# Optimization experiments

Hardware: AMD Instinct MI355X
Metric: run time of the kernel (lower is better)

## Reference

```python
import jax, jax.numpy as jnp
import numpy as np

IN_DIM = 3
GRID_LEVEL = 7
FEAT_DIMS = 2
HIDDEN = 128
BOUND = 1.0
W0_SINE = 56.0  # n_levels**feature_dims - n_levels = 8**2 - 8
N = 131072


def setup_inputs() -> dict:
    key = jax.random.key(0)
    ks = jax.random.split(key, 10)
    return {
        "in_pos": jax.random.uniform(ks[0], (N, IN_DIM), jnp.float32, -1.0, 1.0),
        "grid_feats": jax.random.uniform(ks[1], (N, IN_DIM + GRID_LEVEL * FEAT_DIMS), jnp.float32),
        "ffn_A": jax.random.normal(ks[2], (GRID_LEVEL, FEAT_DIMS, HIDDEN), jnp.float32) * 5.0,
        "ffn_sigma": jnp.ones((GRID_LEVEL,), jnp.float32),
        "W0": jax.random.uniform(ks[3], (HIDDEN, IN_DIM), jnp.float32, -1.0 / IN_DIM, 1.0 / IN_DIM),
        "b0": jax.random.uniform(ks[4], (HIDDEN,), jnp.float32, -1.0 / IN_DIM, 1.0 / IN_DIM),
        "W_mid": jax.random.uniform(ks[5], (GRID_LEVEL, HIDDEN, HIDDEN), jnp.float32) * (2.0 * np.sqrt(6.0 / HIDDEN) / W0_SINE) - np.sqrt(6.0 / HIDDEN) / W0_SINE,
        "b_mid": jnp.zeros((GRID_LEVEL, HIDDEN), jnp.float32),
        "W_high": jax.random.uniform(ks[6], (GRID_LEVEL, HIDDEN, HIDDEN), jnp.float32) * (2.0 * np.sqrt(6.0 / HIDDEN) / W0_SINE) - np.sqrt(6.0 / HIDDEN) / W0_SINE,
        "b_high": jnp.zeros((GRID_LEVEL, HIDDEN), jnp.float32),
    }


def reference(in_pos, grid_feats, ffn_A, ffn_sigma, W0, b0, W_mid, b_mid, W_high, b_high):
    x = in_pos / BOUND                     # [N, 3], in [-1, 1]
    pos01 = (in_pos + BOUND) / (2.0 * BOUND)  # [N, 3], in [0, 1]

    # grid branch: slice off the first in_dim columns, reshape to [L, N, F]
    gx = grid_feats[..., IN_DIM:].reshape(-1, GRID_LEVEL, FEAT_DIMS).transpose(1, 0, 2)
    A = ffn_A * ffn_sigma[:, None, None]   # [L, F, H]
    grid_x = jnp.sin(jnp.einsum('lnf,lfh->lnh', gx, (2.0 * jnp.pi) * A))  # [L, N, H]

    # first SIREN layer
    x = jnp.sin(W0_SINE * (x @ W0.T + b0))  # [N, H]

    def step(carry, layer):
        x, buf = carry
        Wm, bm, Wh, bh, g = layer
        x = jnp.sin(W0_SINE * (x @ Wm.T + bm))
        x = g + x                                  # residual add of grid features
        buf = buf + jnp.sin(W0_SINE * (x @ Wh.T + bh))  # high-freq accumulation
        return (x, buf), None

    buf0 = jnp.zeros((x.shape[0], HIDDEN), x.dtype)
    (_, buf), _ = jax.lax.scan(step, (x, buf0), (W_mid, b_mid, W_high, b_high, grid_x))

    return jnp.concatenate([pos01, buf / GRID_LEVEL], axis=-1)  # [N, 3 + 128]
```

## Files before the change

### kernel.cpp

```cpp
#include <hip/hip_runtime.h>
#include <hip/hip_bf16.h>


typedef __bf16 bf16_t;
typedef __attribute__((ext_vector_type(8))) __bf16 bf16x8;
typedef __attribute__((ext_vector_type(4))) float f32x4;
typedef __attribute__((ext_vector_type(16))) float f32x16;

#define C56R 8.9126768f
#define INV7 0.14285714285714285f

#define OFF_WMF   0
#define OFF_WMFLO 229376
#define OFF_WHF   458752
#define OFF_EPM   688128

union ChunkU { bf16x8 v; unsigned int d[4]; };

__device__ __forceinline__ unsigned short bfbits(float x) {
  bf16_t b = (bf16_t)x;
  return __builtin_bit_cast(unsigned short, b);
}
__device__ __forceinline__ float bf2f(unsigned short u) {
  return __builtin_bit_cast(float, (unsigned int)u << 16);
}
__device__ __forceinline__ void pack2(float v0, float v1,
                                      unsigned int& ph, unsigned int& pl) {
  unsigned short h0 = bfbits(v0), h1 = bfbits(v1);
  ph = (unsigned int)h0 | ((unsigned int)h1 << 16);
  float l0 = v0 - bf2f(h0), l1 = v1 - bf2f(h1);
  pl = (unsigned int)bfbits(l0) | ((unsigned int)bfbits(l1) << 16);
}
__device__ __forceinline__ void stage16(const void* g, void* l) {
  __builtin_amdgcn_global_load_lds(
      (const __attribute__((address_space(1))) unsigned int*)g,
      (__attribute__((address_space(3))) unsigned int*)l, 16, 0, 0);
}

__global__ void ffb_prep(const float* __restrict__ ffnA, const float* __restrict__ sigma,
                         const float* __restrict__ Wm, const float* __restrict__ bm,
                         const float* __restrict__ Wh, const float* __restrict__ bh,
                         unsigned char* __restrict__ ws) {
  int i = blockIdx.x * 256 + threadIdx.x;
  bf16_t* wmf = (bf16_t*)(ws + OFF_WMF);
  bf16_t* wml = (bf16_t*)(ws + OFF_WMFLO);
  bf16_t* whf = (bf16_t*)(ws + OFF_WHF);
  {
    int j    = i & 7;
    int lane = (i >> 3) & 63;
    int kc   = (i >> 9) & 7;
    int mt   = (i >> 12) & 3;
    int it   = i >> 14;
    int ho   = (mt << 5) + (lane & 31);
    int hin  = (kc << 4) + ((lane >> 5) << 3) + j;
    int src  = (it << 14) + (ho << 7) + hin;
    float w  = Wm[src];
    bf16_t h = (bf16_t)w;
    wmf[i] = h;
    wml[i] = (bf16_t)(w - (float)h);
    whf[i] = (bf16_t)Wh[src];
  }
  if (i < 896) {
    int r  = i & 15;
    int mt = (i >> 4) & 3;
    int hf = (i >> 6) & 1;
    int it = i >> 7;
    int h  = (mt << 5) + (r & 3) + ((r >> 2) << 3) + (hf << 2);
    float sg = sigma[it];
    f32x4 e;
    e.x = ffnA[it * 256 + h] * sg;
    e.y = ffnA[it * 256 + 128 + h] * sg;
    e.z = C56R * bm[it * 128 + h];
    e.w = C56R * bh[it * 128 + h];
    ((f32x4*)(ws + OFF_EPM))[i] = e;
  }
}

__launch_bounds__(512, 4)
__global__ void ffb_main(const float* __restrict__ pos,
                         const float* __restrict__ gfeat,
                         const float* __restrict__ W0,
                         const float* __restrict__ b0,
                         const unsigned char* __restrict__ ws,
                         float* __restrict__ out) {
  __shared__ __align__(16) unsigned char smem[65536];

  const int tid  = threadIdx.x;
  const int L    = tid & 63;
  const int wave = tid >> 6;
  const int qd   = wave >> 2;
  const int sub  = wave & 3;
  const int p    = L & 31;
  const int hf   = L >> 5;
  const int n    = (blockIdx.x << 6) + (qd << 5) + p;

  unsigned char* sMH = smem;
  unsigned char* sX  = smem + 32768 + (qd << 14);

  const bf16_t* __restrict__ WML = (const bf16_t*)(ws + OFF_WMFLO);
  const bf16_t* __restrict__ WHF = (const bf16_t*)(ws + OFF_WHF);
  const f32x4*  __restrict__ EPM = (const f32x4*)(ws + OFF_EPM);
  const float*  __restrict__ EPW = (const float*)(ws + OFF_EPM);

  {
    const unsigned char* src = ws + OFF_WMF + (wave << 12) + (L << 4);
    unsigned char* dst = sMH + (wave << 12);
    #pragma unroll
    for (int c = 0; c < 4; ++c)
      stage16(src + (c << 10), dst + (c << 10));
  }

  const float p0 = pos[n * 3 + 0], p1 = pos[n * 3 + 1], p2 = pos[n * 3 + 2];
  if (sub == 0 && hf == 0) {
    out[n * 131 + 0] = (p0 + 1.f) * 0.5f;
    out[n * 131 + 1] = (p1 + 1.f) * 0.5f;
    out[n * 131 + 2] = (p2 + 1.f) * 0.5f;
  }

  #pragma unroll
  for (int cc = 0; cc < 2; ++cc) {
    const int c = (sub << 1) + cc;
    ChunkU chi, clo;
    #pragma unroll
    for (int jp = 0; jp < 4; ++jp) {
      int h0 = (c << 4) + (hf << 3) + 2 * jp;
      float d0 = __builtin_fmaf(p2, W0[h0*3+2], __builtin_fmaf(p1, W0[h0*3+1], p0 * W0[h0*3+0]));
      float d1 = __builtin_fmaf(p2, W0[h0*3+5], __builtin_fmaf(p1, W0[h0*3+4], p0 * W0[h0*3+3]));
      float v0 = __builtin_amdgcn_sinf(C56R * (d0 + b0[h0]));
      float v1 = __builtin_amdgcn_sinf(C56R * (d1 + b0[h0 + 1]));
      pack2(v0, v1, chi.d[jp], clo.d[jp]);
    }
    *(bf16x8*)(sX + (c << 10) + (L << 4))        = chi.v;
    *(bf16x8*)(sX + 8192 + (c << 10) + (L << 4)) = clo.v;
  }
  __syncthreads();

  f32x16 buf;
  #pragma unroll
  for (int r = 0; r < 16; ++r) buf[r] = 0.f;

  for (int it = 0; it < 8; ++it) {
    if (it > 0) {
      f32x16 acc;
      #pragma unroll
      for (int r = 0; r < 16; ++r) acc[r] = 0.f;
      const bf16_t* wb = WHF + ((it - 1) << 14) + (sub << 12) + (L << 3);
      bf16x8 fnext = *(const bf16x8*)(wb);
      #pragma unroll
      for (int kc = 0; kc < 8; ++kc) {
        bf16x8 f = fnext;
        if (kc < 7) fnext = *(const bf16x8*)(wb + ((kc + 1) << 9));
        bf16x8 xhc = *(const bf16x8*)(sX + (kc << 10) + (L << 4));
        acc = __builtin_amdgcn_mfma_f32_32x32x16_bf16(f, xhc, acc, 0, 0, 0);
      }
      const int eb = ((((it - 1) << 1) + hf) << 2) + sub;
      #pragma unroll
      for (int r = 0; r < 16; ++r) {
        float cbh = EPW[(eb * 16 + r) * 4 + 3];
        buf[r] += __builtin_amdgcn_sinf(__builtin_fmaf(acc[r], C56R, cbh));
      }
    }

    if (it < 7) {
      f32x16 acc;
      #pragma unroll
      for (int r = 0; r < 16; ++r) acc[r] = 0.f;
      const bf16_t* wl = WML + (it << 14) + (sub << 12) + (L << 3);
      const unsigned char* smh = sMH + (sub << 13) + (L << 4);
      bf16x8 flnext = *(const bf16x8*)(wl);
      #pragma unroll
      for (int kc = 0; kc < 8; ++kc) {
        bf16x8 fl = flnext;
        if (kc < 7) flnext = *(const bf16x8*)(wl + ((kc + 1) << 9));
        bf16x8 fh  = *(const bf16x8*)(smh + (kc << 10));
        bf16x8 xhc = *(const bf16x8*)(sX + (kc << 10) + (L << 4));
        bf16x8 xlc = *(const bf16x8*)(sX + 8192 + (kc << 10) + (L << 4));
        acc = __builtin_amdgcn_mfma_f32_32x32x16_bf16(fh, xhc, acc, 0, 0, 0);
        acc = __builtin_amdgcn_mfma_f32_32x32x16_bf16(fl, xhc, acc, 0, 0, 0);
        acc = __builtin_amdgcn_mfma_f32_32x32x16_bf16(fh, xlc, acc, 0, 0, 0);
      }

      __syncthreads();

      if (it < 6) {
        const unsigned char* src = ws + OFF_WMF + ((it + 1) << 15) + (wave << 12) + (L << 4);
        unsigned char* dst = sMH + (wave << 12);
        #pragma unroll
        for (int c = 0; c < 4; ++c)
          stage16(src + (c << 10), dst + (c << 10));
      }

      const float g0 = gfeat[n * 17 + 3 + 2 * it];
      const float g1 = gfeat[n * 17 + 4 + 2 * it];
      const int eb = (((it << 1) + hf) << 2) + sub;
      #pragma unroll
      for (int rp = 0; rp < 8; ++rp) {
        const int r = 2 * rp;
        f32x4 e0 = EPM[eb * 16 + r];
        f32x4 e1 = EPM[eb * 16 + r + 1];
        float sg0 = __builtin_amdgcn_sinf(__builtin_amdgcn_fractf(__builtin_fmaf(g1, e0.y, g0 * e0.x)));
        float sg1 = __builtin_amdgcn_sinf(__builtin_amdgcn_fractf(__builtin_fmaf(g1, e1.y, g0 * e1.x)));
        float sm0 = __builtin_amdgcn_sinf(__builtin_fmaf(acc[r],     C56R, e0.z));
        float sm1 = __builtin_amdgcn_sinf(__builtin_fmaf(acc[r + 1], C56R, e1.z));
        unsigned int phv, plv;
        pack2(sg0 + sm0, sg1 + sm1, phv, plv);
        const int h   = (sub << 5) + (r & 3) + ((r >> 2) << 3) + (hf << 2);
        const int off = ((h >> 4) << 10) + ((p + (((h >> 3) & 1) << 5)) << 4) + ((h & 7) << 1);
        *(unsigned int*)(sX + off)        = phv;
        *(unsigned int*)(sX + 8192 + off) = plv;
      }
      __syncthreads();
    }
  }

  float* op = out + (size_t)n * 131 + 3;
  #pragma unroll
  for (int r = 0; r < 16; ++r) {
    const int h = (sub << 5) + (r & 3) + ((r >> 2) << 3) + (hf << 2);
    op[h] = buf[r] * INV7;
  }
}

extern "C" void kernel_launch(void* const* d_in, const int* in_sizes, int n_in,
                              void* d_out, int out_size, void* d_ws, size_t ws_size,
                              hipStream_t stream) {
  (void)in_sizes; (void)n_in; (void)out_size; (void)ws_size;
  const float* pos   = (const float*)d_in[0];
  const float* gfeat = (const float*)d_in[1];
  const float* ffnA  = (const float*)d_in[2];
  const float* sigma = (const float*)d_in[3];
  const float* W0    = (const float*)d_in[4];
  const float* b0    = (const float*)d_in[5];
  const float* Wm    = (const float*)d_in[6];
  const float* bm    = (const float*)d_in[7];
  const float* Wh    = (const float*)d_in[8];
  const float* bh    = (const float*)d_in[9];
  float* out = (float*)d_out;
  unsigned char* ws = (unsigned char*)d_ws;

  hipLaunchKernelGGL(ffb_prep, dim3(448), dim3(256), 0, stream,
                     ffnA, sigma, Wm, bm, Wh, bh, ws);
  hipLaunchKernelGGL(ffb_main, dim3(2048), dim3(512), 0, stream,
                     pos, gfeat, W0, b0, ws, out);
}
```

Measured before the change: 284.3 us.

## Keep activations in registers with each wave owning all output rows for 32 points

Each wave now computes all 128 hidden outputs for its own 32 points, so the activations stay in registers across layers instead of round-tripping through shared memory. The hi and lo mid-layer weights are both staged in LDS, and the bf16 activation fragments are rebuilt with permlane32 swaps between lanes. Blocks now cover 256 points, so the grid drops to 512 blocks and occupancy is lowered to 2 blocks per CU. The cost is much higher register pressure (four accumulators plus the x fragments and buf), which may cause spills or lower occupancy.

```diff
diff --git a/kernel.cpp b/kernel.cpp
--- a/kernel.cpp
+++ b/kernel.cpp
@@ -76,148 +76,164 @@
   }
 }
 
-__launch_bounds__(512, 4)
+__launch_bounds__(512, 2)
 __global__ void ffb_main(const float* __restrict__ pos,
                          const float* __restrict__ gfeat,
                          const float* __restrict__ W0,
                          const float* __restrict__ b0,
                          const unsigned char* __restrict__ ws,
                          float* __restrict__ out) {
-  __shared__ __align__(16) unsigned char smem[65536];
+  __shared__ __align__(16) unsigned char sW[65536];
 
   const int tid  = threadIdx.x;
   const int L    = tid & 63;
   const int wave = tid >> 6;
-  const int qd   = wave >> 2;
-  const int sub  = wave & 3;
   const int p    = L & 31;
   const int hf   = L >> 5;
-  const int n    = (blockIdx.x << 6) + (qd << 5) + p;
-
-  unsigned char* sMH = smem;
-  unsigned char* sX  = smem + 32768 + (qd << 14);
-
-  const bf16_t* __restrict__ WML = (const bf16_t*)(ws + OFF_WMFLO);
+  const int n    = (blockIdx.x << 8) + (wave << 5) + p;
+
   const bf16_t* __restrict__ WHF = (const bf16_t*)(ws + OFF_WHF);
   const f32x4*  __restrict__ EPM = (const f32x4*)(ws + OFF_EPM);
   const float*  __restrict__ EPW = (const float*)(ws + OFF_EPM);
 
   {
-    const unsigned char* src = ws + OFF_WMF + (wave << 12) + (L << 4);
-    unsigned char* dst = sMH + (wave << 12);
-    #pragma unroll
-    for (int c = 0; c < 4; ++c)
-      stage16(src + (c << 10), dst + (c << 10));
+    const unsigned char* srcb = ws + (wave < 4 ? OFF_WMF : OFF_WMFLO)
+                              + ((wave & 3) << 13) + (L << 4);
+    unsigned char* dstb = sW + ((wave >> 2) << 15) + ((wave & 3) << 13);
+    #pragma unroll
+    for (int c = 0; c < 8; ++c)
+      stage16(srcb + (c << 10), dstb + (c << 10));
   }
 
   const float p0 = pos[n * 3 + 0], p1 = pos[n * 3 + 1], p2 = pos[n * 3 + 2];
-  if (sub == 0 && hf == 0) {
-    out[n * 131 + 0] = (p0 + 1.f) * 0.5f;
-    out[n * 131 + 1] = (p1 + 1.f) * 0.5f;
-    out[n * 131 + 2] = (p2 + 1.f) * 0.5f;
-  }
-
+  if (hf == 0) {
+    out[(size_t)n * 131 + 0] = (p0 + 1.f) * 0.5f;
+    out[(size_t)n * 131 + 1] = (p1 + 1.f) * 0.5f;
+    out[(size_t)n * 131 + 2] = (p2 + 1.f) * 0.5f;
+  }
+
+  bf16x8 xh[8], xl[8];
   #pragma unroll
-  for (int cc = 0; cc < 2; ++cc) {
-    const int c = (sub << 1) + cc;
+  for (int kc = 0; kc < 8; ++kc) {
     ChunkU chi, clo;
     #pragma unroll
     for (int jp = 0; jp < 4; ++jp) {
-      int h0 = (c << 4) + (hf << 3) + 2 * jp;
+      const int h0 = (kc << 4) + (hf << 3) + 2 * jp;
       float d0 = __builtin_fmaf(p2, W0[h0*3+2], __builtin_fmaf(p1, W0[h0*3+1], p0 * W0[h0*3+0]));
       float d1 = __builtin_fmaf(p2, W0[h0*3+5], __builtin_fmaf(p1, W0[h0*3+4], p0 * W0[h0*3+3]));
       float v0 = __builtin_amdgcn_sinf(C56R * (d0 + b0[h0]));
       float v1 = __builtin_amdgcn_sinf(C56R * (d1 + b0[h0 + 1]));
       pack2(v0, v1, chi.d[jp], clo.d[jp]);
     }
-    *(bf16x8*)(sX + (c << 10) + (L << 4))        = chi.v;
-    *(bf16x8*)(sX + 8192 + (c << 10) + (L << 4)) = clo.v;
-  }
+    xh[kc] = chi.v;
+    xl[kc] = clo.v;
+  }
+
+  f32x16 buf[4];
+  #pragma unroll
+  for (int mt = 0; mt < 4; ++mt)
+    #pragma unroll
+    for (int r = 0; r < 16; ++r) buf[mt][r] = 0.f;
+
   __syncthreads();
 
-  f32x16 buf;
-  #pragma unroll
-  for (int r = 0; r < 16; ++r) buf[r] = 0.f;
-
-  for (int it = 0; it < 8; ++it) {
-    if (it > 0) {
-      f32x16 acc;
-      #pragma unroll
-      for (int r = 0; r < 16; ++r) acc[r] = 0.f;
-      const bf16_t* wb = WHF + ((it - 1) << 14) + (sub << 12) + (L << 3);
-      bf16x8 fnext = *(const bf16x8*)(wb);
-      #pragma unroll
-      for (int kc = 0; kc < 8; ++kc) {
-        bf16x8 f = fnext;
-        if (kc < 7) fnext = *(const bf16x8*)(wb + ((kc + 1) << 9));
-        bf16x8 xhc = *(const bf16x8*)(sX + (kc << 10) + (L << 4));
-        acc = __builtin_amdgcn_mfma_f32_32x32x16_bf16(f, xhc, acc, 0, 0, 0);
-      }
-      const int eb = ((((it - 1) << 1) + hf) << 2) + sub;
+  #pragma unroll 1
+  for (int l = 0; l < 7; ++l) {
+    f32x16 acc[4];
+    #pragma unroll
+    for (int mt = 0; mt < 4; ++mt)
+      #pragma unroll
+      for (int r = 0; r < 16; ++r) acc[mt][r] = 0.f;
+
+    #pragma unroll
+    for (int kc = 0; kc < 8; ++kc) {
+      #pragma unroll
+      for (int mt = 0; mt < 4; ++mt) {
+        const bf16x8 fh = *(const bf16x8*)(sW + (mt << 13) + (kc << 10) + (L << 4));
+        const bf16x8 fl = *(const bf16x8*)(sW + 32768 + (mt << 13) + (kc << 10) + (L << 4));
+        acc[mt] = __builtin_amdgcn_mfma_f32_32x32x16_bf16(fh, xh[kc], acc[mt], 0, 0, 0);
+        acc[mt] = __builtin_amdgcn_mfma_f32_32x32x16_bf16(fl, xh[kc], acc[mt], 0, 0, 0);
+        acc[mt] = __builtin_amdgcn_mfma_f32_32x32x16_bf16(fh, xl[kc], acc[mt], 0, 0, 0);
+      }
+    }
+    __syncthreads();
+
+    if (l < 6) {
+      const unsigned char* srcb = ws + (wave < 4 ? OFF_WMF : OFF_WMFLO)
+                                + ((l + 1) << 15) + ((wave & 3) << 13) + (L << 4);
+      unsigned char* dstb = sW + ((wave >> 2) << 15) + ((wave & 3) << 13);
+      #pragma unroll
+      for (int c = 0; c < 8; ++c)
+        stage16(srcb + (c << 10), dstb + (c << 10));
+    }
+
+    const float g0 = gfeat[n * 17 + 3 + 2 * l];
+    const float g1 = gfeat[n * 17 + 4 + 2 * l];
+    #pragma unroll
+    for (int mt = 0; mt < 4; ++mt) {
+      const int eb = (((l << 1) + hf) << 2) + mt;
+      float v[16];
       #pragma unroll
       for (int r = 0; r < 16; ++r) {
-        float cbh = EPW[(eb * 16 + r) * 4 + 3];
-        buf[r] += __builtin_amdgcn_sinf(__builtin_fmaf(acc[r], C56R, cbh));
-      }
-    }
-
-    if (it < 7) {
-      f32x16 acc;
-      #pragma unroll
-      for (int r = 0; r < 16; ++r) acc[r] = 0.f;
-      const bf16_t* wl = WML + (it << 14) + (sub << 12) + (L << 3);
-      const unsigned char* smh = sMH + (sub << 13) + (L << 4);
-      bf16x8 flnext = *(const bf16x8*)(wl);
-      #pragma unroll
-      for (int kc = 0; kc < 8; ++kc) {
-        bf16x8 fl = flnext;
-        if (kc < 7) flnext = *(const bf16x8*)(wl + ((kc + 1) << 9));
-        bf16x8 fh  = *(const bf16x8*)(smh + (kc << 10));
-        bf16x8 xhc = *(const bf16x8*)(sX + (kc << 10) + (L << 4));
-        bf16x8 xlc = *(const bf16x8*)(sX + 8192 + (kc << 10) + (L << 4));
-        acc = __builtin_amdgcn_mfma_f32_32x32x16_bf16(fh, xhc, acc, 0, 0, 0);
-        acc = __builtin_amdgcn_mfma_f32_32x32x16_bf16(fl, xhc, acc, 0, 0, 0);
-        acc = __builtin_amdgcn_mfma_f32_32x32x16_bf16(fh, xlc, acc, 0, 0, 0);
-      }
-
-      __syncthreads();
-
-      if (it < 6) {
-        const unsigned char* src = ws + OFF_WMF + ((it + 1) << 15) + (wave << 12) + (L << 4);
-        unsigned char* dst = sMH + (wave << 12);
-        #pragma unroll
-        for (int c = 0; c < 4; ++c)
-          stage16(src + (c << 10), dst + (c << 10));
-      }
-
-      const float g0 = gfeat[n * 17 + 3 + 2 * it];
-      const float g1 = gfeat[n * 17 + 4 + 2 * it];
-      const int eb = (((it << 1) + hf) << 2) + sub;
-      #pragma unroll
-      for (int rp = 0; rp < 8; ++rp) {
-        const int r = 2 * rp;
-        f32x4 e0 = EPM[eb * 16 + r];
-        f32x4 e1 = EPM[eb * 16 + r + 1];
-        float sg0 = __builtin_amdgcn_sinf(__builtin_amdgcn_fractf(__builtin_fmaf(g1, e0.y, g0 * e0.x)));
-        float sg1 = __builtin_amdgcn_sinf(__builtin_amdgcn_fractf(__builtin_fmaf(g1, e1.y, g0 * e1.x)));
-        float sm0 = __builtin_amdgcn_sinf(__builtin_fmaf(acc[r],     C56R, e0.z));
-        float sm1 = __builtin_amdgcn_sinf(__builtin_fmaf(acc[r + 1], C56R, e1.z));
-        unsigned int phv, plv;
-        pack2(sg0 + sm0, sg1 + sm1, phv, plv);
-        const int h   = (sub << 5) + (r & 3) + ((r >> 2) << 3) + (hf << 2);
-        const int off = ((h >> 4) << 10) + ((p + (((h >> 3) & 1) << 5)) << 4) + ((h & 7) << 1);
-        *(unsigned int*)(sX + off)        = phv;
-        *(unsigned int*)(sX + 8192 + off) = plv;
-      }
-      __syncthreads();
-    }
+        const f32x4 e = EPM[eb * 16 + r];
+        const float sg = __builtin_amdgcn_sinf(__builtin_amdgcn_fractf(__builtin_fmaf(g1, e.y, g0 * e.x)));
+        const float sm = __builtin_amdgcn_sinf(__builtin_fmaf(acc[mt][r], C56R, e.z));
+        v[r] = sg + sm;
+      }
+      #pragma unroll
+      for (int bh = 0; bh < 2; ++bh) {
+        unsigned int Ah, Al, Bh, Bl, Ch, Cl, Dh, Dl;
+        pack2(v[8*bh + 0], v[8*bh + 1], Ah, Al);
+        pack2(v[8*bh + 2], v[8*bh + 3], Bh, Bl);
+        pack2(v[8*bh + 4], v[8*bh + 5], Ch, Cl);
+        pack2(v[8*bh + 6], v[8*bh + 7], Dh, Dl);
+        asm("v_permlane32_swap_b32 %0, %1" : "+v"(Ah), "+v"(Ch));
+        asm("v_permlane32_swap_b32 %0, %1" : "+v"(Bh), "+v"(Dh));
+        asm("v_permlane32_swap_b32 %0, %1" : "+v"(Al), "+v"(Cl));
+        asm("v_permlane32_swap_b32 %0, %1" : "+v"(Bl), "+v"(Dl));
+        ChunkU uh, ul;
+        uh.d[0] = Ah; uh.d[1] = Bh; uh.d[2] = Ch; uh.d[3] = Dh;
+        ul.d[0] = Al; ul.d[1] = Bl; ul.d[2] = Cl; ul.d[3] = Dl;
+        xh[2*mt + bh] = uh.v;
+        xl[2*mt + bh] = ul.v;
+      }
+    }
+
+    f32x16 hac[4];
+    #pragma unroll
+    for (int mt = 0; mt < 4; ++mt)
+      #pragma unroll
+      for (int r = 0; r < 16; ++r) hac[mt][r] = 0.f;
+
+    const bf16_t* whb = WHF + (l << 14) + (L << 3);
+    #pragma unroll
+    for (int kc = 0; kc < 8; ++kc) {
+      #pragma unroll
+      for (int mt = 0; mt < 4; ++mt) {
+        const bf16x8 f = *(const bf16x8*)(whb + (mt << 12) + (kc << 9));
+        hac[mt] = __builtin_amdgcn_mfma_f32_32x32x16_bf16(f, xh[kc], hac[mt], 0, 0, 0);
+      }
+    }
+    #pragma unroll
+    for (int mt = 0; mt < 4; ++mt) {
+      const int eb = (((l << 1) + hf) << 2) + mt;
+      #pragma unroll
+      for (int r = 0; r < 16; ++r) {
+        const float cbh = EPW[(eb * 16 + r) * 4 + 3];
+        buf[mt][r] += __builtin_amdgcn_sinf(__builtin_fmaf(hac[mt][r], C56R, cbh));
+      }
+    }
+    __syncthreads();
   }
 
   float* op = out + (size_t)n * 131 + 3;
   #pragma unroll
-  for (int r = 0; r < 16; ++r) {
-    const int h = (sub << 5) + (r & 3) + ((r >> 2) << 3) + (hf << 2);
-    op[h] = buf[r] * INV7;
+  for (int mt = 0; mt < 4; ++mt) {
+    #pragma unroll
+    for (int r = 0; r < 16; ++r) {
+      const int h = (mt << 5) + (r & 3) + ((r >> 2) << 3) + (hf << 2);
+      op[h] = buf[mt][r] * INV7;
+    }
   }
 }
 
@@ -240,6 +256,6 @@
 
   hipLaunchKernelGGL(ffb_prep, dim3(448), dim3(256), 0, stream,
                      ffnA, sigma, Wm, bm, Wh, bh, ws);
-  hipLaunchKernelGGL(ffb_main, dim3(2048), dim3(512), 0, stream,
+  hipLaunchKernelGGL(ffb_main, dim3(512), dim3(512), 0, stream,
                      pos, gfeat, W0, b0, ws, out);
 }
```

Measured after the change: 369.2 us. 29.9% more time.

## Drop LDS staging of mid-layer weights and halve block size

Applied to the files above, without the earlier changes.

Removes the async global-to-LDS staging of the high-part mid-layer weights and loads them directly from global memory into registers with a one-step register prefetch, like the low part. Blocks shrink from 512 to 256 threads (one 32-point group per block), LDS drops from 64KB to 16KB, and the launch bound moves to 8 blocks per CU to raise occupancy. This trades the LDS weight sharing across two point groups for more global/L2 weight traffic per block and extra register pressure from the second prefetch stream.

```diff
diff --git a/kernel.cpp b/kernel.cpp
--- a/kernel.cpp
+++ b/kernel.cpp
@@ -30,11 +30,6 @@
   ph = (unsigned int)h0 | ((unsigned int)h1 << 16);
   float l0 = v0 - bf2f(h0), l1 = v1 - bf2f(h1);
   pl = (unsigned int)bfbits(l0) | ((unsigned int)bfbits(l1) << 16);
-}
-__device__ __forceinline__ void stage16(const void* g, void* l) {
-  __builtin_amdgcn_global_load_lds(
-      (const __attribute__((address_space(1))) unsigned int*)g,
-      (__attribute__((address_space(3))) unsigned int*)l, 16, 0, 0);
 }
 
 __global__ void ffb_prep(const float* __restrict__ ffnA, const float* __restrict__ sigma,
@@ -76,45 +71,33 @@
   }
 }
 
-__launch_bounds__(512, 4)
+__launch_bounds__(256, 8)
 __global__ void ffb_main(const float* __restrict__ pos,
                          const float* __restrict__ gfeat,
                          const float* __restrict__ W0,
                          const float* __restrict__ b0,
                          const unsigned char* __restrict__ ws,
                          float* __restrict__ out) {
-  __shared__ __align__(16) unsigned char smem[65536];
+  __shared__ __align__(16) unsigned char sX[16384];
 
   const int tid  = threadIdx.x;
   const int L    = tid & 63;
-  const int wave = tid >> 6;
-  const int qd   = wave >> 2;
-  const int sub  = wave & 3;
+  const int sub  = tid >> 6;
   const int p    = L & 31;
   const int hf   = L >> 5;
-  const int n    = (blockIdx.x << 6) + (qd << 5) + p;
-
-  unsigned char* sMH = smem;
-  unsigned char* sX  = smem + 32768 + (qd << 14);
-
+  const int n    = (blockIdx.x << 5) + p;
+
+  const bf16_t* __restrict__ WMH = (const bf16_t*)(ws + OFF_WMF);
   const bf16_t* __restrict__ WML = (const bf16_t*)(ws + OFF_WMFLO);
   const bf16_t* __restrict__ WHF = (const bf16_t*)(ws + OFF_WHF);
   const f32x4*  __restrict__ EPM = (const f32x4*)(ws + OFF_EPM);
   const float*  __restrict__ EPW = (const float*)(ws + OFF_EPM);
 
-  {
-    const unsigned char* src = ws + OFF_WMF + (wave << 12) + (L << 4);
-    unsigned char* dst = sMH + (wave << 12);
-    #pragma unroll
-    for (int c = 0; c < 4; ++c)
-      stage16(src + (c << 10), dst + (c << 10));
-  }
-
   const float p0 = pos[n * 3 + 0], p1 = pos[n * 3 + 1], p2 = pos[n * 3 + 2];
   if (sub == 0 && hf == 0) {
-    out[n * 131 + 0] = (p0 + 1.f) * 0.5f;
-    out[n * 131 + 1] = (p1 + 1.f) * 0.5f;
-    out[n * 131 + 2] = (p2 + 1.f) * 0.5f;
+    out[(size_t)n * 131 + 0] = (p0 + 1.f) * 0.5f;
+    out[(size_t)n * 131 + 1] = (p1 + 1.f) * 0.5f;
+    out[(size_t)n * 131 + 2] = (p2 + 1.f) * 0.5f;
   }
 
   #pragma unroll
@@ -165,14 +148,18 @@
       f32x16 acc;
       #pragma unroll
       for (int r = 0; r < 16; ++r) acc[r] = 0.f;
+      const bf16_t* wh = WMH + (it << 14) + (sub << 12) + (L << 3);
       const bf16_t* wl = WML + (it << 14) + (sub << 12) + (L << 3);
-      const unsigned char* smh = sMH + (sub << 13) + (L << 4);
+      bf16x8 fhnext = *(const bf16x8*)(wh);
       bf16x8 flnext = *(const bf16x8*)(wl);
       #pragma unroll
       for (int kc = 0; kc < 8; ++kc) {
+        bf16x8 fh = fhnext;
         bf16x8 fl = flnext;
-        if (kc < 7) flnext = *(const bf16x8*)(wl + ((kc + 1) << 9));
-        bf16x8 fh  = *(const bf16x8*)(smh + (kc << 10));
+        if (kc < 7) {
+          fhnext = *(const bf16x8*)(wh + ((kc + 1) << 9));
+          flnext = *(const bf16x8*)(wl + ((kc + 1) << 9));
+        }
         bf16x8 xhc = *(const bf16x8*)(sX + (kc << 10) + (L << 4));
         bf16x8 xlc = *(const bf16x8*)(sX + 8192 + (kc << 10) + (L << 4));
         acc = __builtin_amdgcn_mfma_f32_32x32x16_bf16(fh, xhc, acc, 0, 0, 0);
@@ -181,14 +168,6 @@
       }
 
       __syncthreads();
-
-      if (it < 6) {
-        const unsigned char* src = ws + OFF_WMF + ((it + 1) << 15) + (wave << 12) + (L << 4);
-        unsigned char* dst = sMH + (wave << 12);
-        #pragma unroll
-        for (int c = 0; c < 4; ++c)
-          stage16(src + (c << 10), dst + (c << 10));
-      }
 
       const float g0 = gfeat[n * 17 + 3 + 2 * it];
       const float g1 = gfeat[n * 17 + 4 + 2 * it];
@@ -240,6 +219,6 @@
 
   hipLaunchKernelGGL(ffb_prep, dim3(448), dim3(256), 0, stream,
                      ffnA, sigma, Wm, bm, Wh, bh, ws);
-  hipLaunchKernelGGL(ffb_main, dim3(2048), dim3(512), 0, stream,
+  hipLaunchKernelGGL(ffb_main, dim3(4096), dim3(256), 0, stream,
                      pos, gfeat, W0, b0, ws, out);
 }
```

New measurement: 347.9 us. 22.4% more time.
